# Optimization experiments

Measured on AMD Instinct MI355X. Metric: run time of the kernel, lower is better.

The kernel has to match this reference:

```python
import jax, jax.numpy as jnp
import numpy as np

HIDDEN = 1024
OUT = 8192
N_SUBJ = 8
B = 64
T = 512


def setup_inputs() -> dict:
    key = jax.random.key(0)
    ks = jax.random.split(key, 12)
    s = 1.0 / np.sqrt(HIDDEN)
    return {
        "context": jax.random.normal(ks[0], (B, T, HIDDEN), dtype=jnp.float32),
        "subject_ids": jax.random.randint(ks[1], (B,), 0, N_SUBJ),
        "eps": jax.random.normal(ks[2], (B, OUT), dtype=jnp.float32),
        # pool_proj: Linear(H,H) -> GELU -> Linear(H,H); weights stored (in,out)
        "w1": jax.random.normal(ks[3], (HIDDEN, HIDDEN), dtype=jnp.float32) * s,
        "b1": jax.random.normal(ks[4], (HIDDEN,), dtype=jnp.float32) * s,
        "w2": jax.random.normal(ks[5], (HIDDEN, HIDDEN), dtype=jnp.float32) * s,
        "b2": jax.random.normal(ks[6], (HIDDEN,), dtype=jnp.float32) * s,
        # SubjectLayers params, init normal(0, 1/sqrt(in))
        "subj_w": jax.random.normal(ks[7], (N_SUBJ, HIDDEN, OUT), dtype=jnp.float32) * s,
        "subj_b": jax.random.normal(ks[8], (N_SUBJ, OUT), dtype=jnp.float32) * s,
        # log_var head: weight std 1e-4, bias -2.0
        "lv_w": jax.random.normal(ks[9], (HIDDEN, OUT), dtype=jnp.float32) * 1e-4,
        "lv_b": jnp.full((OUT,), -2.0, dtype=jnp.float32),
    }


def reference(context, subject_ids, eps, w1, b1, w2, b2, subj_w, subj_b, lv_w, lv_b):
    # mean-pool over time: (B,T,H) -> (B,H)
    h = context.mean(axis=1)
    # pool_proj MLP with exact GELU (torch default)
    h = jax.nn.gelu(h @ w1 + b1, approximate=False) @ w2 + b2
    # per-subject linear head: gather (H,OUT) weight per sample, matvec
    w = subj_w[subject_ids]            # (B, H, OUT)
    mu = jnp.einsum("bd,bdo->bo", h, w) + subj_b[subject_ids]
    # variational log-variance head, clamped
    log_var = jnp.clip(h @ lv_w + lv_b, -10.0, 2.0)
    # reparameterized sample (training mode)
    x0 = mu + eps * jnp.exp(0.5 * log_var)
    return x0, mu, log_var
```

## Files before the change

### kernel.cpp

```cpp
#include <hip/hip_runtime.h>
#include <math.h>

#define HID   1024
#define OUTD  8192
#define NSUBJ 8
#define BATCH 64
#define TLEN  512

#define OFF_PP    0u
#define OFF_P1    1048576u
#define OFF_P2    3145728u
#define OFF_H     5242880u
#define OFF_MUP   5308416u
#define OFF_LVP   9502720u

__global__ __launch_bounds__(256) void k_pool(const float* __restrict__ ctx,
                                              float* __restrict__ pp) {
    int b  = blockIdx.x;
    int tc = blockIdx.y;
    int hid = threadIdx.x * 4;
    const float* base = ctx + ((size_t)b * TLEN + (size_t)tc * 32) * HID + hid;
    float4 acc = make_float4(0.f, 0.f, 0.f, 0.f);
#pragma unroll 8
    for (int t = 0; t < 32; ++t) {
        float4 v = *(const float4*)(base + (size_t)t * HID);
        acc.x += v.x; acc.y += v.y; acc.z += v.z; acc.w += v.w;
    }
    *(float4*)(pp + ((size_t)tc * BATCH + b) * HID + hid) = acc;
}

__global__ __launch_bounds__(256) void k_mlp1(const float* __restrict__ pp,
                                              const float* __restrict__ w1,
                                              float* __restrict__ p1) {
    __shared__ float xs[32][34];
    int j  = blockIdx.x * 256 + threadIdx.x;
    int k0 = blockIdx.y * 32;
    int b0 = blockIdx.z * 32;
    {
        int bb = threadIdx.x >> 3;
        int kk = (threadIdx.x & 7) * 4;
        float4 s = make_float4(0.f, 0.f, 0.f, 0.f);
#pragma unroll
        for (int tc = 0; tc < 16; ++tc) {
            float4 v = *(const float4*)(pp + (size_t)tc * 65536 + (b0 + bb) * 1024 + k0 + kk);
            s.x += v.x; s.y += v.y; s.z += v.z; s.w += v.w;
        }
        const float inv = 1.0f / 512.0f;
        xs[bb][kk]     = s.x * inv;
        xs[bb][kk + 1] = s.y * inv;
        xs[bb][kk + 2] = s.z * inv;
        xs[bb][kk + 3] = s.w * inv;
    }
    __syncthreads();
    float acc[32];
#pragma unroll
    for (int i = 0; i < 32; ++i) acc[i] = 0.f;
    for (int kk = 0; kk < 32; kk += 2) {
        float wa = w1[(size_t)(k0 + kk) * HID + j];
        float wb = w1[(size_t)(k0 + kk + 1) * HID + j];
#pragma unroll
        for (int i = 0; i < 32; ++i) {
            acc[i] = fmaf(xs[i][kk], wa, acc[i]);
            acc[i] = fmaf(xs[i][kk + 1], wb, acc[i]);
        }
    }
    float* dst = p1 + (size_t)blockIdx.y * 65536;
#pragma unroll
    for (int i = 0; i < 32; ++i) dst[(b0 + i) * 1024 + j] = acc[i];
}

__global__ __launch_bounds__(256) void k_mlp2(const float* __restrict__ p1,
                                              const float* __restrict__ b1,
                                              const float* __restrict__ w2,
                                              float* __restrict__ p2) {
    __shared__ float xs[32][34];
    int j  = blockIdx.x * 256 + threadIdx.x;
    int k0 = blockIdx.y * 32;
    int b0 = blockIdx.z * 32;
    {
        int bb = threadIdx.x >> 3;
        int kk = (threadIdx.x & 7) * 4;
        float4 s = make_float4(0.f, 0.f, 0.f, 0.f);
#pragma unroll
        for (int kc = 0; kc < 32; ++kc) {
            float4 v = *(const float4*)(p1 + (size_t)kc * 65536 + (b0 + bb) * 1024 + k0 + kk);
            s.x += v.x; s.y += v.y; s.z += v.z; s.w += v.w;
        }
        float4 bbv = *(const float4*)(b1 + k0 + kk);
        s.x += bbv.x; s.y += bbv.y; s.z += bbv.z; s.w += bbv.w;
        const float r = 0.70710678118654752f;
        xs[bb][kk]     = 0.5f * s.x * (1.0f + erff(s.x * r));
        xs[bb][kk + 1] = 0.5f * s.y * (1.0f + erff(s.y * r));
        xs[bb][kk + 2] = 0.5f * s.z * (1.0f + erff(s.z * r));
        xs[bb][kk + 3] = 0.5f * s.w * (1.0f + erff(s.w * r));
    }
    __syncthreads();
    float acc[32];
#pragma unroll
    for (int i = 0; i < 32; ++i) acc[i] = 0.f;
    for (int kk = 0; kk < 32; kk += 2) {
        float wa = w2[(size_t)(k0 + kk) * HID + j];
        float wb = w2[(size_t)(k0 + kk + 1) * HID + j];
#pragma unroll
        for (int i = 0; i < 32; ++i) {
            acc[i] = fmaf(xs[i][kk], wa, acc[i]);
            acc[i] = fmaf(xs[i][kk + 1], wb, acc[i]);
        }
    }
    float* dst = p2 + (size_t)blockIdx.y * 65536;
#pragma unroll
    for (int i = 0; i < 32; ++i) dst[(b0 + i) * 1024 + j] = acc[i];
}

__global__ __launch_bounds__(256) void k_red_bias(const float* __restrict__ p,
                                                  const float* __restrict__ bias,
                                                  float* __restrict__ out) {
    int i = (blockIdx.x * 256 + threadIdx.x) * 4;
    int j = i & (HID - 1);
    float4 s = make_float4(0.f, 0.f, 0.f, 0.f);
#pragma unroll
    for (int kc = 0; kc < 32; ++kc) {
        float4 v = *(const float4*)(p + (size_t)kc * 65536 + i);
        s.x += v.x; s.y += v.y; s.z += v.z; s.w += v.w;
    }
    float4 bb = *(const float4*)(bias + j);
    s.x += bb.x; s.y += bb.y; s.z += bb.z; s.w += bb.w;
    *(float4*)(out + i) = s;
}

template <int NS, int KLEN>
__device__ __forceinline__ void mu_tile(const float* __restrict__ hmat,
                                        const float* __restrict__ wbase,
                                        float* __restrict__ dst_kc,
                                        const int* bo, int n, int k0, int o) {
    float4 acc[NS];
#pragma unroll
    for (int i = 0; i < NS; ++i) acc[i] = make_float4(0.f, 0.f, 0.f, 0.f);
    float4 wv[4];
#pragma unroll
    for (int kk = 0; kk < 4; ++kk)
        wv[kk] = *(const float4*)(wbase + (size_t)(k0 + kk) * OUTD + o);
    for (int k = k0; k < k0 + KLEN; k += 4) {
        float4 hv[NS];
#pragma unroll
        for (int i = 0; i < NS; ++i)
            hv[i] = *(const float4*)(hmat + bo[i] * HID + k);
        int kn = (k + 4 < k0 + KLEN) ? (k + 4) : k0;
        float4 wn[4];
#pragma unroll
        for (int kk = 0; kk < 4; ++kk)
            wn[kk] = *(const float4*)(wbase + (size_t)(kn + kk) * OUTD + o);
#pragma unroll
        for (int kk = 0; kk < 4; ++kk) {
            float4 w = wv[kk];
#pragma unroll
            for (int i = 0; i < NS; ++i) {
                float h = (kk == 0) ? hv[i].x : (kk == 1) ? hv[i].y
                        : (kk == 2) ? hv[i].z : hv[i].w;
                acc[i].x = fmaf(h, w.x, acc[i].x);
                acc[i].y = fmaf(h, w.y, acc[i].y);
                acc[i].z = fmaf(h, w.z, acc[i].z);
                acc[i].w = fmaf(h, w.w, acc[i].w);
            }
        }
#pragma unroll
        for (int kk = 0; kk < 4; ++kk) wv[kk] = wn[kk];
    }
#pragma unroll
    for (int i = 0; i < NS; ++i)
        if (i < n) *(float4*)(dst_kc + (size_t)bo[i] * OUTD + o) = acc[i];
}

__global__ __launch_bounds__(256) void k_head(const float* __restrict__ hbuf,
                                              const float* __restrict__ subj_w,
                                              const float* __restrict__ lv_w,
                                              const int* __restrict__ sid,
                                              float* __restrict__ mup,
                                              float* __restrict__ lvp) {
    int blk = blockIdx.x;
    int tid = threadIdx.x;
    if (blk < 512) {
        int o  = (blk & 7) * 1024 + tid * 4;
        int k0 = ((blk >> 3) & 7) * 128;
        int s  = blk >> 6;
        int lane = tid & 63;
        int mysid = sid[lane];
        unsigned long long m = __ballot(mysid == s);
        int ns = __popcll(m);
        if (ns == 0) return;
        const float* wbase = subj_w + (size_t)s * HID * OUTD;
        float* mup_kc = mup + (size_t)((blk >> 3) & 7) * BATCH * OUTD;
        unsigned long long mm = m;
        for (int base = 0; base < ns; base += 12) {
            int take = ns - base; if (take > 12) take = 12;
            int fb = (int)__builtin_ctzll(mm);
            int bo[12];
#pragma unroll
            for (int i = 0; i < 12; ++i) {
                bo[i] = (mm != 0ull) ? (int)__builtin_ctzll(mm) : fb;
                if (mm != 0ull) mm &= (mm - 1ull);
            }
            if (take <= 4)       mu_tile<4, 128>(hbuf, wbase, mup_kc, bo, take, k0, o);
            else if (take <= 8)  mu_tile<8, 128>(hbuf, wbase, mup_kc, bo, take, k0, o);
            else                 mu_tile<12, 128>(hbuf, wbase, mup_kc, bo, take, k0, o);
        }
    } else {
        int u   = blk - 512;
        int wid = tid >> 6;
        int lane = tid & 63;
        int o  = (u & 31) * 256 + lane * 4;
        int k0 = (u >> 5) * 64;
        int s0 = wid * 16;
        int bo[16];
#pragma unroll
        for (int i = 0; i < 16; ++i) bo[i] = s0 + i;
        float* lvp_kc = lvp + (size_t)(u >> 5) * BATCH * OUTD;
        mu_tile<16, 64>(hbuf, lv_w, lvp_kc, bo, 16, k0, o);
    }
}

__global__ __launch_bounds__(256) void k_combine(const float* __restrict__ mup,
                                                 const float* __restrict__ lvp,
                                                 const float* __restrict__ eps,
                                                 const float* __restrict__ subj_b,
                                                 const float* __restrict__ lv_b,
                                                 const int* __restrict__ sid,
                                                 float* __restrict__ out) {
    int idx = (blockIdx.x * 256 + threadIdx.x) * 4;
    int b = idx >> 13;
    int o = idx & (OUTD - 1);
    float4 m = make_float4(0.f, 0.f, 0.f, 0.f);
    float4 l = make_float4(0.f, 0.f, 0.f, 0.f);
#pragma unroll
    for (int kc = 0; kc < 8; ++kc) {
        float4 t = *(const float4*)(mup + (size_t)kc * 524288 + idx);
        m.x += t.x; m.y += t.y; m.z += t.z; m.w += t.w;
    }
#pragma unroll
    for (int kc = 0; kc < 16; ++kc) {
        float4 u = *(const float4*)(lvp + (size_t)kc * 524288 + idx);
        l.x += u.x; l.y += u.y; l.z += u.z; l.w += u.w;
    }
    int s = sid[b];
    float4 sb = *(const float4*)(subj_b + s * OUTD + o);
    float4 lb = *(const float4*)(lv_b + o);
    m.x += sb.x; m.y += sb.y; m.z += sb.z; m.w += sb.w;
    l.x = fminf(fmaxf(l.x + lb.x, -10.f), 2.f);
    l.y = fminf(fmaxf(l.y + lb.y, -10.f), 2.f);
    l.z = fminf(fmaxf(l.z + lb.z, -10.f), 2.f);
    l.w = fminf(fmaxf(l.w + lb.w, -10.f), 2.f);
    float4 e = *(const float4*)(eps + idx);
    float4 x0;
    x0.x = m.x + e.x * __expf(0.5f * l.x);
    x0.y = m.y + e.y * __expf(0.5f * l.y);
    x0.z = m.z + e.z * __expf(0.5f * l.z);
    x0.w = m.w + e.w * __expf(0.5f * l.w);
    *(float4*)(out + idx) = x0;
    *(float4*)(out + 524288 + idx) = m;
    *(float4*)(out + 1048576 + idx) = l;
}

extern "C" void kernel_launch(void* const* d_in, const int* in_sizes, int n_in,
                              void* d_out, int out_size, void* d_ws, size_t ws_size,
                              hipStream_t stream) {
    const float* ctx    = (const float*)d_in[0];
    const int*   sid    = (const int*)  d_in[1];
    const float* eps    = (const float*)d_in[2];
    const float* w1     = (const float*)d_in[3];
    const float* b1     = (const float*)d_in[4];
    const float* w2     = (const float*)d_in[5];
    const float* b2     = (const float*)d_in[6];
    const float* subj_w = (const float*)d_in[7];
    const float* subj_b = (const float*)d_in[8];
    const float* lv_w   = (const float*)d_in[9];
    const float* lv_b   = (const float*)d_in[10];
    float* out = (float*)d_out;

    float* ws   = (float*)d_ws;
    float* pp   = ws + OFF_PP;
    float* p1   = ws + OFF_P1;
    float* p2   = ws + OFF_P2;
    float* hbuf = ws + OFF_H;
    float* mup  = ws + OFF_MUP;
    float* lvp  = ws + OFF_LVP;

    k_pool<<<dim3(BATCH, 16), 256, 0, stream>>>(ctx, pp);
    k_mlp1<<<dim3(4, 32, 2), 256, 0, stream>>>(pp, w1, p1);
    k_mlp2<<<dim3(4, 32, 2), 256, 0, stream>>>(p1, b1, w2, p2);
    k_red_bias<<<64, 256, 0, stream>>>(p2, b2, hbuf);
    k_head<<<1024, 256, 0, stream>>>(hbuf, subj_w, lv_w, sid, mup, lvp);
    k_combine<<<512, 256, 0, stream>>>(mup, lvp, eps, subj_b, lv_b, sid, out);
}
```

Baseline: 176.0 us.

## Drop split-K partial buffers in pool/MLP and shrink log-var split count

Pooling now reduces over time inside each block through shared memory and writes the mean directly, removing the partial-sum buffer. The two MLP layers become a single templated full-K kernel that applies bias (and GELU) in place, so the separate reduction kernel and large partial buffers go away. The log-var head uses longer K chunks (256 instead of 64), so fewer partials are written and the combine step sums 4 slices instead of 16. The cost is much lower parallelism in the FC kernels (64 blocks) and fewer head blocks, which may underuse the GPU.

```diff
diff --git a/kernel.cpp b/kernel.cpp
--- a/kernel.cpp
+++ b/kernel.cpp
@@ -7,125 +7,82 @@
 #define BATCH 64
 #define TLEN  512
 
-#define OFF_PP    0u
-#define OFF_P1    1048576u
-#define OFF_P2    3145728u
-#define OFF_H     5242880u
-#define OFF_MUP   5308416u
-#define OFF_LVP   9502720u
+#define OFF_H0    0u
+#define OFF_G     65536u
+#define OFF_H     131072u
+#define OFF_MUP   196608u
+#define OFF_LVP   4390912u
 
 __global__ __launch_bounds__(256) void k_pool(const float* __restrict__ ctx,
-                                              float* __restrict__ pp) {
+                                              float* __restrict__ h0) {
     int b  = blockIdx.x;
-    int tc = blockIdx.y;
-    int hid = threadIdx.x * 4;
-    const float* base = ctx + ((size_t)b * TLEN + (size_t)tc * 32) * HID + hid;
+    int hc = blockIdx.y;
+    int col  = threadIdx.x & 31;
+    int toct = threadIdx.x >> 5;
+    const float* base = ctx + ((size_t)b * TLEN + (size_t)toct * 64) * HID
+                        + hc * 128 + col * 4;
     float4 acc = make_float4(0.f, 0.f, 0.f, 0.f);
 #pragma unroll 8
-    for (int t = 0; t < 32; ++t) {
+    for (int t = 0; t < 64; ++t) {
         float4 v = *(const float4*)(base + (size_t)t * HID);
         acc.x += v.x; acc.y += v.y; acc.z += v.z; acc.w += v.w;
     }
-    *(float4*)(pp + ((size_t)tc * BATCH + b) * HID + hid) = acc;
-}
-
-__global__ __launch_bounds__(256) void k_mlp1(const float* __restrict__ pp,
-                                              const float* __restrict__ w1,
-                                              float* __restrict__ p1) {
-    __shared__ float xs[32][34];
-    int j  = blockIdx.x * 256 + threadIdx.x;
-    int k0 = blockIdx.y * 32;
-    int b0 = blockIdx.z * 32;
-    {
-        int bb = threadIdx.x >> 3;
-        int kk = (threadIdx.x & 7) * 4;
+    __shared__ float4 sm[8][32];
+    sm[toct][col] = acc;
+    __syncthreads();
+    if (threadIdx.x < 32) {
         float4 s = make_float4(0.f, 0.f, 0.f, 0.f);
 #pragma unroll
-        for (int tc = 0; tc < 16; ++tc) {
-            float4 v = *(const float4*)(pp + (size_t)tc * 65536 + (b0 + bb) * 1024 + k0 + kk);
+        for (int r = 0; r < 8; ++r) {
+            float4 v = sm[r][threadIdx.x];
             s.x += v.x; s.y += v.y; s.z += v.z; s.w += v.w;
         }
         const float inv = 1.0f / 512.0f;
-        xs[bb][kk]     = s.x * inv;
-        xs[bb][kk + 1] = s.y * inv;
-        xs[bb][kk + 2] = s.z * inv;
-        xs[bb][kk + 3] = s.w * inv;
-    }
-    __syncthreads();
-    float acc[32];
-#pragma unroll
-    for (int i = 0; i < 32; ++i) acc[i] = 0.f;
-    for (int kk = 0; kk < 32; kk += 2) {
-        float wa = w1[(size_t)(k0 + kk) * HID + j];
-        float wb = w1[(size_t)(k0 + kk + 1) * HID + j];
-#pragma unroll
-        for (int i = 0; i < 32; ++i) {
-            acc[i] = fmaf(xs[i][kk], wa, acc[i]);
-            acc[i] = fmaf(xs[i][kk + 1], wb, acc[i]);
-        }
-    }
-    float* dst = p1 + (size_t)blockIdx.y * 65536;
-#pragma unroll
-    for (int i = 0; i < 32; ++i) dst[(b0 + i) * 1024 + j] = acc[i];
-}
-
-__global__ __launch_bounds__(256) void k_mlp2(const float* __restrict__ p1,
-                                              const float* __restrict__ b1,
-                                              const float* __restrict__ w2,
-                                              float* __restrict__ p2) {
-    __shared__ float xs[32][34];
-    int j  = blockIdx.x * 256 + threadIdx.x;
-    int k0 = blockIdx.y * 32;
-    int b0 = blockIdx.z * 32;
-    {
-        int bb = threadIdx.x >> 3;
-        int kk = (threadIdx.x & 7) * 4;
-        float4 s = make_float4(0.f, 0.f, 0.f, 0.f);
-#pragma unroll
-        for (int kc = 0; kc < 32; ++kc) {
-            float4 v = *(const float4*)(p1 + (size_t)kc * 65536 + (b0 + bb) * 1024 + k0 + kk);
-            s.x += v.x; s.y += v.y; s.z += v.z; s.w += v.w;
-        }
-        float4 bbv = *(const float4*)(b1 + k0 + kk);
-        s.x += bbv.x; s.y += bbv.y; s.z += bbv.z; s.w += bbv.w;
-        const float r = 0.70710678118654752f;
-        xs[bb][kk]     = 0.5f * s.x * (1.0f + erff(s.x * r));
-        xs[bb][kk + 1] = 0.5f * s.y * (1.0f + erff(s.y * r));
-        xs[bb][kk + 2] = 0.5f * s.z * (1.0f + erff(s.z * r));
-        xs[bb][kk + 3] = 0.5f * s.w * (1.0f + erff(s.w * r));
-    }
-    __syncthreads();
-    float acc[32];
-#pragma unroll
-    for (int i = 0; i < 32; ++i) acc[i] = 0.f;
-    for (int kk = 0; kk < 32; kk += 2) {
-        float wa = w2[(size_t)(k0 + kk) * HID + j];
-        float wb = w2[(size_t)(k0 + kk + 1) * HID + j];
-#pragma unroll
-        for (int i = 0; i < 32; ++i) {
-            acc[i] = fmaf(xs[i][kk], wa, acc[i]);
-            acc[i] = fmaf(xs[i][kk + 1], wb, acc[i]);
-        }
-    }
-    float* dst = p2 + (size_t)blockIdx.y * 65536;
-#pragma unroll
-    for (int i = 0; i < 32; ++i) dst[(b0 + i) * 1024 + j] = acc[i];
-}
-
-__global__ __launch_bounds__(256) void k_red_bias(const float* __restrict__ p,
-                                                  const float* __restrict__ bias,
-                                                  float* __restrict__ out) {
-    int i = (blockIdx.x * 256 + threadIdx.x) * 4;
-    int j = i & (HID - 1);
-    float4 s = make_float4(0.f, 0.f, 0.f, 0.f);
-#pragma unroll
-    for (int kc = 0; kc < 32; ++kc) {
-        float4 v = *(const float4*)(p + (size_t)kc * 65536 + i);
-        s.x += v.x; s.y += v.y; s.z += v.z; s.w += v.w;
-    }
-    float4 bb = *(const float4*)(bias + j);
-    s.x += bb.x; s.y += bb.y; s.z += bb.z; s.w += bb.w;
-    *(float4*)(out + i) = s;
+        s.x *= inv; s.y *= inv; s.z *= inv; s.w *= inv;
+        *(float4*)(h0 + (size_t)b * HID + hc * 128 + threadIdx.x * 4) = s;
+    }
+}
+
+template <bool GELU>
+__global__ __launch_bounds__(256) void k_fc(const float* __restrict__ x,
+                                            const float* __restrict__ w,
+                                            const float* __restrict__ bias,
+                                            float* __restrict__ y) {
+    __shared__ float xs[32][66];
+    int j  = blockIdx.x * 32 + (threadIdx.x & 31);
+    int b0 = blockIdx.y * 32;
+    int bl = threadIdx.x >> 5;
+    float acc[4] = {0.f, 0.f, 0.f, 0.f};
+    for (int kc = 0; kc < 16; ++kc) {
+        int k0 = kc * 64;
+        __syncthreads();
+        {
+            int idx = threadIdx.x * 2;
+            int r  = idx >> 4;
+            int c4 = idx & 15;
+            const float* src = x + (size_t)(b0 + r) * HID + k0 + c4 * 4;
+            float4 v0 = *(const float4*)(src);
+            float4 v1 = *(const float4*)(src + 4);
+            *(float4*)&xs[r][c4 * 4]     = v0;
+            *(float4*)&xs[r][c4 * 4 + 4] = v1;
+        }
+        __syncthreads();
+#pragma unroll 8
+        for (int k = 0; k < 64; ++k) {
+            float wv = w[(size_t)(k0 + k) * HID + j];
+#pragma unroll
+            for (int s = 0; s < 4; ++s)
+                acc[s] = fmaf(xs[bl + s * 8][k], wv, acc[s]);
+        }
+    }
+    float bv = bias[j];
+#pragma unroll
+    for (int s = 0; s < 4; ++s) {
+        int b = b0 + bl + s * 8;
+        float v = acc[s] + bv;
+        if (GELU) v = 0.5f * v * (1.0f + erff(v * 0.70710678118654752f));
+        y[(size_t)b * HID + j] = v;
+    }
 }
 
 template <int NS, int KLEN>
@@ -209,13 +166,13 @@
         int wid = tid >> 6;
         int lane = tid & 63;
         int o  = (u & 31) * 256 + lane * 4;
-        int k0 = (u >> 5) * 64;
+        int k0 = (u >> 5) * 256;
         int s0 = wid * 16;
         int bo[16];
 #pragma unroll
         for (int i = 0; i < 16; ++i) bo[i] = s0 + i;
         float* lvp_kc = lvp + (size_t)(u >> 5) * BATCH * OUTD;
-        mu_tile<16, 64>(hbuf, lv_w, lvp_kc, bo, 16, k0, o);
+        mu_tile<16, 256>(hbuf, lv_w, lvp_kc, bo, 16, k0, o);
     }
 }
 
@@ -237,7 +194,7 @@
         m.x += t.x; m.y += t.y; m.z += t.z; m.w += t.w;
     }
 #pragma unroll
-    for (int kc = 0; kc < 16; ++kc) {
+    for (int kc = 0; kc < 4; ++kc) {
         float4 u = *(const float4*)(lvp + (size_t)kc * 524288 + idx);
         l.x += u.x; l.y += u.y; l.z += u.z; l.w += u.w;
     }
@@ -277,17 +234,15 @@
     float* out = (float*)d_out;
 
     float* ws   = (float*)d_ws;
-    float* pp   = ws + OFF_PP;
-    float* p1   = ws + OFF_P1;
-    float* p2   = ws + OFF_P2;
+    float* h0   = ws + OFF_H0;
+    float* g    = ws + OFF_G;
     float* hbuf = ws + OFF_H;
     float* mup  = ws + OFF_MUP;
     float* lvp  = ws + OFF_LVP;
 
-    k_pool<<<dim3(BATCH, 16), 256, 0, stream>>>(ctx, pp);
-    k_mlp1<<<dim3(4, 32, 2), 256, 0, stream>>>(pp, w1, p1);
-    k_mlp2<<<dim3(4, 32, 2), 256, 0, stream>>>(p1, b1, w2, p2);
-    k_red_bias<<<64, 256, 0, stream>>>(p2, b2, hbuf);
-    k_head<<<1024, 256, 0, stream>>>(hbuf, subj_w, lv_w, sid, mup, lvp);
+    k_pool<<<dim3(BATCH, 8), 256, 0, stream>>>(ctx, h0);
+    k_fc<true><<<dim3(32, 2), 256, 0, stream>>>(h0, w1, b1, g);
+    k_fc<false><<<dim3(32, 2), 256, 0, stream>>>(g, w2, b2, hbuf);
+    k_head<<<640, 256, 0, stream>>>(hbuf, subj_w, lv_w, sid, mup, lvp);
     k_combine<<<512, 256, 0, stream>>>(mup, lvp, eps, subj_b, lv_b, sid, out);
 }
```

Result: slower. 309.7 us (+76.0%).
